# Kernel optimization log

Measured on AMD Instinct MI355X. Metric: run time of the kernel, lower is better.

The kernel has to match this reference:

```python
import jax, jax.numpy as jnp
import numpy as np

NUM_BOXES = 16384
NUM_CLASS = 3
CODE_SIZE = 7
NMS_PRE = 1024
NMS_POST = 512
NMS_THRESH = 0.8
EPS = 1e-8


def _cross(a, b):
    return a[..., 0] * b[..., 1] - a[..., 1] * b[..., 0]


def _bev_corners(b5):
    # b5: (..., 5) = (cx, cy, dx, dy, ry) -> corners (..., 4, 2)
    c, s = jnp.cos(b5[..., 4]), jnp.sin(b5[..., 4])
    off = jnp.array([[0.5, 0.5], [-0.5, 0.5], [-0.5, -0.5], [0.5, -0.5]], dtype=b5.dtype)
    lx = b5[..., 2:3] * off[:, 0]  # (..., 4)
    ly = b5[..., 3:4] * off[:, 1]
    cx = b5[..., 0:1] + lx * c[..., None] - ly * s[..., None]
    cy = b5[..., 1:2] + lx * s[..., None] + ly * c[..., None]
    return jnp.stack([cx, cy], axis=-1)


def _points_in_box(p, b5):
    # p: (..., K, 2), b5: (..., 5) -> (..., K) bool (point inside rotated rect)
    c, s = jnp.cos(b5[..., 4:5]), jnp.sin(b5[..., 4:5])
    rel = p - b5[..., None, 0:2]
    qx = rel[..., 0] * c + rel[..., 1] * s
    qy = -rel[..., 0] * s + rel[..., 1] * c
    return (jnp.abs(qx) <= b5[..., 2:3] * 0.5 + 1e-5) & (jnp.abs(qy) <= b5[..., 3:4] * 0.5 + 1e-5)


def _pairwise_bev_iou(b5):
    # b5: (N, 5) -> (N, N) rotated BEV IoU (matches iou3d nms_gpu's BEV IoU)
    a = b5[:, None, :]
    b = b5[None, :, :]
    ca = _bev_corners(a)  # (N,1,4,2)
    cb = _bev_corners(b)  # (1,N,4,2)
    # edge-edge segment intersections: (N,N,4,4)
    a0, da = ca, jnp.roll(ca, -1, axis=-2) - ca
    b0, db = cb, jnp.roll(cb, -1, axis=-2) - cb
    A0, DA = a0[..., :, None, :], da[..., :, None, :]
    B0, DB = b0[..., None, :, :], db[..., None, :, :]
    den = _cross(DA, DB)
    d = B0 - A0
    den_s = jnp.where(jnp.abs(den) > EPS, den, 1.0)
    t = _cross(d, DB) / den_s
    u = _cross(d, DA) / den_s
    ok = (jnp.abs(den) > EPS) & (t >= 0) & (t <= 1) & (u >= 0) & (u <= 1)
    p_ee = A0 + t[..., None] * DA  # (N,N,4,4,2)
    shp = p_ee.shape[:-3]
    p_ee = p_ee.reshape(shp + (16, 2))
    ok = ok.reshape(shp + (16,))
    in_b = _points_in_box(ca, b)  # corners of A inside B: (N,N,4)
    in_a = _points_in_box(cb, a)  # corners of B inside A: (N,N,4)
    pts = jnp.concatenate([p_ee,
                           jnp.broadcast_to(ca, shp + (4, 2)),
                           jnp.broadcast_to(cb, shp + (4, 2))], axis=-2)  # (N,N,24,2)
    msk = jnp.concatenate([ok, in_b, in_a], axis=-1)  # (N,N,24)
    # order candidate vertices by angle around centroid (intersection is convex)
    cnt = jnp.maximum(msk.sum(-1, keepdims=True), 1)
    ctr = (pts * msk[..., None]).sum(-2, keepdims=True) / cnt[..., None]  # (N,N,1,2)
    ang = jnp.arctan2(pts[..., 1] - ctr[..., 1], pts[..., 0] - ctr[..., 0])
    ang = jnp.where(msk, ang, 1e9)  # invalid points sorted to the end
    order = jnp.argsort(ang, axis=-1)
    pts_s = jnp.take_along_axis(pts, order[..., None], axis=-2)
    msk_s = jnp.take_along_axis(msk, order, axis=-1)
    first = pts_s[..., 0:1, :]
    poly = jnp.where(msk_s[..., None], pts_s, first)  # pad with first vertex (zero shoelace contribution)
    inter = 0.5 * jnp.abs(_cross(poly, jnp.roll(poly, -1, axis=-2)).sum(-1))
    area_a = a[..., 2] * a[..., 3]
    area_b = b[..., 2] * b[..., 3]
    return inter / jnp.maximum(area_a + area_b - inter, 1e-6)


def _greedy_nms(iou, thresh):
    n = iou.shape[0]
    idx = jnp.arange(n)

    def body(i, supp):
        alive = jnp.logical_not(supp[i])
        return supp | (alive & (iou[i] > thresh) & (idx > i))

    supp = jax.lax.fori_loop(0, n, body, jnp.zeros((n,), dtype=bool))
    return ~supp


def _select_one(box_preds, cls_preds):
    # box_preds: (M, 7), cls_preds: (M, C) -> padded selected indices + validity
    scores = jnp.max(cls_preds, axis=1)
    _, top_idx = jax.lax.top_k(scores, NMS_PRE)  # score-descending, like torch.topk
    bev = box_preds[top_idx][:, jnp.array([0, 1, 3, 4, 6])]  # (cx,cy,dx,dy,ry)
    iou = _pairwise_bev_iou(bev)
    keep = _greedy_nms(iou, NMS_THRESH)
    pri = jnp.where(keep, jnp.arange(NMS_PRE), 2 * NMS_PRE)
    pos = jnp.sort(pri)[:NMS_POST]  # kept positions in score order
    valid = pos < NMS_PRE
    sel = top_idx[jnp.minimum(pos, NMS_PRE - 1)]
    return sel, valid


def setup_inputs() -> dict:
    key = jax.random.key(0)
    k1, k2, k3, k4, k5 = jax.random.split(key, 5)
    B = 2
    xy = jax.random.uniform(k1, (B, NUM_BOXES, 2), minval=-50.0, maxval=50.0)
    z = jax.random.uniform(k2, (B, NUM_BOXES, 1), minval=-2.0, maxval=1.0)
    dims = jax.random.uniform(k3, (B, NUM_BOXES, 3), minval=1.0, maxval=5.0)
    ry = jax.random.uniform(k4, (B, NUM_BOXES, 1), minval=-np.pi, maxval=np.pi)
    batch_box_preds = jnp.concatenate([xy, z, dims, ry], axis=-1).astype(jnp.float32)
    batch_cls_preds = (jax.random.normal(k5, (B, NUM_BOXES, NUM_CLASS)) * 3.0).astype(jnp.float32)
    return {"batch_box_preds": batch_box_preds, "batch_cls_preds": batch_cls_preds}


def reference(batch_box_preds, batch_cls_preds):
    # RoIHeadTemplate.proposal_layer: per-sample max-score, class-agnostic NMS,
    # scatter into zero-padded (B, NMS_POST, ...) tensors.
    sel, valid = jax.vmap(_select_one)(batch_box_preds, batch_cls_preds)  # (B, NMS_POST)
    rois = jnp.take_along_axis(batch_box_preds, sel[..., None], axis=1)
    logits = jnp.take_along_axis(batch_cls_preds, sel[..., None], axis=1)
    labels = jnp.argmax(logits, axis=-1)
    scores = jnp.max(logits, axis=-1)
    v = valid[..., None]
    rois = jnp.where(v, rois, 0.0)
    logits = jnp.where(v, logits, 0.0)
    scores = jnp.where(valid, scores, 0.0)
    roi_labels = jnp.where(valid, labels, 0) + 1  # padded slots end up as 1, same as torch (zeros + 1)
    return rois, scores, roi_labels, logits
```

## Files before the change

### kernel.cpp

```cpp
#include <hip/hip_runtime.h>
#include <hip/hip_bf16.h>
#include <math.h>

#define NBOX   16384
#define NPRE   1024
#define NPOST  512
#define NMS_TH 0.8f
#define DEN_EPS 1e-8f
#define NCAND  2048
#define NBUCK  8192

typedef unsigned long long ull;

__device__ __forceinline__ unsigned mono_f32(float a) {
  unsigned u = __float_as_uint(a);
  return (u & 0x80000000u) ? ~u : (u | 0x80000000u);
}

__global__ __launch_bounds__(1024) void k_hist(
    const float* __restrict__ cls, ull* __restrict__ cand,
    unsigned* __restrict__ candCount, unsigned* __restrict__ nz) {
  __shared__ unsigned hist[NBUCK];
  __shared__ unsigned wsuf[16];
  __shared__ unsigned thrT;
  __shared__ unsigned cnt;
  int b = blockIdx.x;
  int t = threadIdx.x;
  int lane = t & 63, wv = t >> 6;
  nz[b * NPRE + t] = 0u;
#pragma unroll
  for (int k = 0; k < NBUCK / 1024; ++k) hist[t + k * 1024] = 0u;
  if (t == 0) cnt = 0u;
  __syncthreads();

  ull key[16];
#pragma unroll
  for (int k = 0; k < 16; ++k) {
    int i = k * 1024 + t;
    const float* cc = cls + ((size_t)b * NBOX + i) * 3;
    float s = fmaxf(cc[0], fmaxf(cc[1], cc[2]));
    unsigned u = mono_f32(s);
    key[k] = ((ull)u << 14) | (ull)(16383 - i);
    atomicAdd(&hist[u >> 19], 1u);
  }
  __syncthreads();

  unsigned s8 = 0;
#pragma unroll
  for (int k = 0; k < 8; ++k) s8 += hist[t * 8 + k];
  unsigned v = s8;
#pragma unroll
  for (int off = 1; off < 64; off <<= 1) {
    unsigned o = __shfl_down(v, off, 64);
    if (lane + off < 64) v += o;
  }
  if (lane == 0) wsuf[wv] = v;
  __syncthreads();
  if (t < 16) {
    unsigned x = wsuf[t];
#pragma unroll
    for (int off = 1; off < 16; off <<= 1) {
      unsigned o = __shfl_down(x, off, 64);
      if (t + off < 16) x += o;
    }
    wsuf[t] = x;
  }
  __syncthreads();
  unsigned Sown = v + ((wv < 15) ? wsuf[wv + 1] : 0u);
  unsigned Snxt = Sown - s8;
  if (Sown >= NPRE && Snxt < NPRE) {
    unsigned c = Snxt;
    unsigned T = t * 8;
    for (int k = 7; k >= 0; --k) {
      c += hist[t * 8 + k];
      if (c >= NPRE) { T = t * 8 + k; break; }
    }
    thrT = T;
  }
  __syncthreads();
  unsigned T = thrT;
#pragma unroll
  for (int k = 0; k < 16; ++k) {
    bool c = (unsigned)(key[k] >> 33) >= T;
    ull bal = __ballot(c);
    if (bal) {
      unsigned base = 0;
      if (lane == 0) base = atomicAdd(&cnt, (unsigned)__popcll(bal));
      base = (unsigned)__shfl((int)base, 0, 64);
      if (c) {
        unsigned pos = base + (unsigned)__popcll(bal & ((1ull << lane) - 1ull));
        if (pos < NCAND) cand[(size_t)b * NCAND + pos] = key[k];
      }
    }
  }
  __syncthreads();
  if (t == 0) candCount[b] = (cnt < NCAND) ? cnt : NCAND;
}

__global__ __launch_bounds__(256) void k_ranksel(
    const float* __restrict__ box, const ull* __restrict__ cand,
    const unsigned* __restrict__ candCount,
    int* __restrict__ topi, float* __restrict__ binfo, float4* __restrict__ pinfo) {
  __shared__ ull lk[NCAND];
  int b = blockIdx.y;
  int tid = threadIdx.x;
  int j = blockIdx.x * 256 + tid;
  unsigned C = candCount[b];
#pragma unroll
  for (int k = 0; k < NCAND / 256; ++k) {
    int idx = k * 256 + tid;
    lk[idx] = ((unsigned)idx < C) ? cand[(size_t)b * NCAND + idx] : 0ULL;
  }
  __syncthreads();
  ull my = ((unsigned)j < C) ? lk[j] : 0ULL;
  int r = 0;
  const ulonglong2* p2 = (const ulonglong2*)lk;
#pragma unroll 8
  for (int k = 0; k < NCAND / 2; ++k) {
    ulonglong2 kk = p2[k];
    r += (kk.x > my) ? 1 : 0;
    r += (kk.y > my) ? 1 : 0;
  }
  if ((unsigned)j >= C || r >= NPRE) return;
  int i = 16383 - (int)(my & 0x3FFFULL);
  topi[b * NPRE + r] = i;
  const float* bp = box + ((size_t)b * NBOX + i) * 7;
  float x = bp[0], y = bp[1], dx = bp[3], dy = bp[4], ry = bp[6];
  float c = cosf(ry), s = sinf(ry);
  float* o = binfo + ((size_t)b * NPRE + r) * 16;
  o[0] = x; o[1] = y; o[2] = dx; o[3] = dy; o[4] = c; o[5] = s;
  const float offx[4] = {0.5f, -0.5f, -0.5f, 0.5f};
  const float offy[4] = {0.5f, 0.5f, -0.5f, -0.5f};
#pragma unroll
  for (int k = 0; k < 4; ++k) {
    float lx = dx * offx[k], ly = dy * offy[k];
    o[6 + k]  = x + lx * c - ly * s;
    o[10 + k] = y + lx * s + ly * c;
  }
  float rad = 0.5f * sqrtf(dx * dx + dy * dy);
  float area = dx * dy;
  o[14] = rad; o[15] = area;
  pinfo[(size_t)b * NPRE + r] = make_float4(x, y, rad, area);
}

__device__ bool iou_exact_gt(const float* __restrict__ Ab, const float* __restrict__ Bb) {
  float ax = Ab[0], ay = Ab[1], bx = Bb[0], by = Bb[1];
  float aA = Ab[15], aB = Bb[15];
  float acx[4], acy[4], bcx[4], bcy[4];
#pragma unroll
  for (int k = 0; k < 4; ++k) {
    acx[k] = Ab[6 + k]; acy[k] = Ab[10 + k];
    bcx[k] = Bb[6 + k]; bcy[k] = Bb[10 + k];
  }
  float px[24], py[24];
  bool act[24];
#pragma unroll
  for (int p = 0; p < 4; ++p) {
    float A0x = acx[p], A0y = acy[p];
    float DAx = acx[(p + 1) & 3] - A0x, DAy = acy[(p + 1) & 3] - A0y;
#pragma unroll
    for (int q = 0; q < 4; ++q) {
      float B0x = bcx[q], B0y = bcy[q];
      float DBx = bcx[(q + 1) & 3] - B0x, DBy = bcy[(q + 1) & 3] - B0y;
      float den = DAx * DBy - DAy * DBx;
      float dxx = B0x - A0x, dyy = B0y - A0y;
      bool dok = fabsf(den) > DEN_EPS;
      float dens = dok ? den : 1.0f;
      float t = (dxx * DBy - dyy * DBx) / dens;
      float u = (dxx * DAy - dyy * DAx) / dens;
      int k = p * 4 + q;
      px[k] = A0x + t * DAx;
      py[k] = A0y + t * DAy;
      act[k] = dok && t >= 0.f && t <= 1.f && u >= 0.f && u <= 1.f;
    }
  }
  float cA = Ab[4], sA = Ab[5], cB = Bb[4], sB = Bb[5];
#pragma unroll
  for (int k = 0; k < 4; ++k) {
    float rx = acx[k] - bx, ry = acy[k] - by;
    float qx =  rx * cB + ry * sB, qy = -rx * sB + ry * cB;
    px[16 + k] = acx[k]; py[16 + k] = acy[k];
    act[16 + k] = (fabsf(qx) <= Bb[2] * 0.5f + 1e-5f) && (fabsf(qy) <= Bb[3] * 0.5f + 1e-5f);
  }
#pragma unroll
  for (int k = 0; k < 4; ++k) {
    float rx = bcx[k] - ax, ry = bcy[k] - ay;
    float qx =  rx * cA + ry * sA, qy = -rx * sA + ry * cA;
    px[20 + k] = bcx[k]; py[20 + k] = bcy[k];
    act[20 + k] = (fabsf(qx) <= Ab[2] * 0.5f + 1e-5f) && (fabsf(qy) <= Ab[3] * 0.5f + 1e-5f);
  }
  int cnt = 0; float sx = 0.f, sy = 0.f;
#pragma unroll
  for (int k = 0; k < 24; ++k)
    if (act[k]) { cnt++; sx += px[k]; sy += py[k]; }
  float fc = (float)(cnt > 1 ? cnt : 1);
  float cx0 = sx / fc, cy0 = sy / fc;
  ull key[24];
#pragma unroll
  for (int k = 0; k < 24; ++k) {
    float ang = atan2f(py[k] - cy0, px[k] - cx0);
    key[k] = act[k] ? ((((ull)mono_f32(ang)) << 5) | (ull)k) : ~0ull;
  }
  ull kmin = ~0ull; float fx = 0.f, fy = 0.f;
#pragma unroll
  for (int k = 0; k < 24; ++k) {
    bool lt = key[k] < kmin;
    kmin = lt ? key[k] : kmin;
    fx = lt ? px[k] : fx;
    fy = lt ? py[k] : fy;
  }
  float ssum = 0.f;
#pragma unroll
  for (int k = 0; k < 24; ++k) {
    ull myk = key[k];
    ull best = ~0ull; float nx = fx, ny = fy;
#pragma unroll
    for (int j = 0; j < 24; ++j) {
      bool c = (key[j] > myk) && (key[j] < best);
      best = c ? key[j] : best;
      nx = c ? px[j] : nx;
      ny = c ? py[j] : ny;
    }
    float contrib = px[k] * ny - py[k] * nx;
    ssum += (myk != ~0ull) ? contrib : 0.f;
  }
  float inter = 0.5f * fabsf(ssum);
  float uni = aA + aB - inter;
  return inter / fmaxf(uni, 1e-6f) > NMS_TH;
}

__global__ __launch_bounds__(256) void k_pairs(
    const float* __restrict__ binfo, const float4* __restrict__ pinfo,
    ull* __restrict__ mask, unsigned* __restrict__ nz) {
  int wv = (blockIdx.x * 256 + threadIdx.x) >> 6;
  int lane = threadIdx.x & 63;
  int w = wv & 15;
  int i = (wv >> 4) & (NPRE - 1);
  int b = wv >> 14;
  if (w * 64 + 63 <= i) return;
  int j = w * 64 + lane;
  float4 pj = pinfo[(size_t)b * NPRE + j];
  float4 pi = pinfo[(size_t)b * NPRE + i];
  bool cand = false;
  if (j > i) {
    float ddx = pi.x - pj.x, ddy = pi.y - pj.y;
    float rr = pi.z + pj.z + 1e-3f;
    if (ddx * ddx + ddy * ddy <= rr * rr) {
      float mn = fminf(pi.w, pj.w), mx = fmaxf(pi.w, pj.w);
      if (mn > NMS_TH * mx) cand = true;
    }
  }
  const float* base = binfo + (size_t)b * NPRE * 16;
  bool pred = cand && iou_exact_gt(base + (size_t)i * 16, base + (size_t)j * 16);
  ull bal = __ballot(pred);
  if (lane == 0 && bal) {
    mask[((size_t)b * NPRE + i) * 16 + w] = bal;
    atomicOr(&nz[b * NPRE + i], 1u << w);
  }
}

__global__ __launch_bounds__(1024) void k_final(
    const float* __restrict__ box, const float* __restrict__ cls,
    const int* __restrict__ topi, const ull* __restrict__ mask,
    const unsigned* __restrict__ nz, float* __restrict__ out, int B) {
  __shared__ ull remv_sh[16];
  int b = blockIdx.x;
  int p = threadIdx.x;
  int lane = p & 63, wid = p >> 6;

  if (wid == 0) {
    ull rfr[16];
#pragma unroll
    for (int w = 0; w < 16; ++w) {
      unsigned vz = nz[b * NPRE + w * 64 + lane];
      rfr[w] = __ballot(vz != 0u);
    }
    ull remv = 0;
    for (int w = 0; w < 16; ++w) {
      ull bb = rfr[w];
      while (bb) {
        int ii = __ffsll(bb) - 1;
        bb &= bb - 1;
        int row = w * 64 + ii;
        ull rw = __shfl(remv, w, 64);
        if (!((rw >> ii) & 1ULL)) {
          unsigned nzi = nz[b * NPRE + row];
          ull m = 0;
          if (lane < 16 && ((nzi >> lane) & 1u))
            m = mask[((size_t)b * NPRE + row) * 16 + lane];
          remv |= m;
        }
      }
    }
    if (lane < 16) remv_sh[lane] = remv;
  }
  __syncthreads();

  ull rw = remv_sh[wid];
  int alive = ((rw >> lane) & 1ULL) ? 0 : 1;
  int v = alive;
#pragma unroll
  for (int off = 1; off < 64; off <<= 1) {
    int t = __shfl_up(v, off, 64);
    if (lane >= off) v += t;
  }
  __shared__ int wtot[16], woff[17];
  if (lane == 63) wtot[wid] = v;
  __syncthreads();
  if (p == 0) {
    int acc = 0;
    for (int t = 0; t < 16; ++t) { woff[t] = acc; acc += wtot[t]; }
    woff[16] = acc;
  }
  __syncthreads();
  int excl = v - alive + woff[wid];
  int total = woff[16];
  float* rois   = out;
  float* scores = out + (size_t)B * NPOST * 7;
  float* labels = scores + (size_t)B * NPOST;
  float* logits = labels + (size_t)B * NPOST;
  if (alive && excl < NPOST) {
    int s = excl;
    int orig = topi[b * NPRE + p];
    const float* bb = box + ((size_t)b * NBOX + orig) * 7;
    float* ro = rois + ((size_t)b * NPOST + s) * 7;
#pragma unroll
    for (int c = 0; c < 7; ++c) ro[c] = bb[c];
    const float* cc = cls + ((size_t)b * NBOX + orig) * 3;
    float l0 = cc[0], l1 = cc[1], l2 = cc[2];
    float m = fmaxf(l0, fmaxf(l1, l2));
    int lab = (l0 == m) ? 0 : ((l1 == m) ? 1 : 2);
    scores[b * NPOST + s] = m;
    labels[b * NPOST + s] = (float)(lab + 1);
    float* lg = logits + ((size_t)b * NPOST + s) * 3;
    lg[0] = l0; lg[1] = l1; lg[2] = l2;
  }
  if (p < NPOST && p >= total) {
    float* ro = rois + ((size_t)b * NPOST + p) * 7;
#pragma unroll
    for (int c = 0; c < 7; ++c) ro[c] = 0.f;
    scores[b * NPOST + p] = 0.f;
    labels[b * NPOST + p] = 1.f;
    float* lg = logits + ((size_t)b * NPOST + p) * 3;
    lg[0] = 0.f; lg[1] = 0.f; lg[2] = 0.f;
  }
}

extern "C" void kernel_launch(void* const* d_in, const int* in_sizes, int n_in,
                              void* d_out, int out_size, void* d_ws, size_t ws_size,
                              hipStream_t stream) {
  const float* box = (const float*)d_in[0];
  const float* cls = (const float*)d_in[1];
  float* out = (float*)d_out;
  int B = in_sizes[0] / (NBOX * 7);

  char* w = (char*)d_ws;
  size_t off = 0;
  ull* cand        = (ull*)(w + off);      off += (size_t)B * NCAND * sizeof(ull);
  unsigned* candCt = (unsigned*)(w + off); off += (size_t)B * sizeof(unsigned);
  int* topi        = (int*)(w + off);      off += (size_t)B * NPRE * sizeof(int);
  off = (off + 63) & ~(size_t)63;
  float* binfo     = (float*)(w + off);    off += (size_t)B * NPRE * 16 * sizeof(float);
  float4* pinfo    = (float4*)(w + off);   off += (size_t)B * NPRE * sizeof(float4);
  ull* mask        = (ull*)(w + off);      off += (size_t)B * NPRE * 16 * sizeof(ull);
  unsigned* nz     = (unsigned*)(w + off); off += (size_t)B * NPRE * sizeof(unsigned);
  (void)off; (void)ws_size; (void)out_size; (void)n_in;

  hipLaunchKernelGGL(k_hist,    dim3(B), dim3(1024), 0, stream, cls, cand, candCt, nz);
  hipLaunchKernelGGL(k_ranksel, dim3(NCAND / 256, B), dim3(256), 0, stream, box, cand, candCt, topi, binfo, pinfo);
  hipLaunchKernelGGL(k_pairs,   dim3(B * NPRE * 16 / 4), dim3(256), 0, stream, binfo, pinfo, mask, nz);
  hipLaunchKernelGGL(k_final,   dim3(B), dim3(1024), 0, stream, box, cls, topi, mask, nz, out, B);
}
```

Before: 157.7 us.

## Fuse top-k, rank-select and pair prefilter into one kernel with worklist NMS

Merges histogram threshold, rank selection and the coarse pair prefilter into a single per-sample kernel. Candidate keys and pinfo now stay in LDS, and pairs that pass the prefilter go to a compact global worklist. The final kernel evaluates exact IoU only on worklist pairs, builds a compact suppression mask in LDS for rows that hit, then runs the serial NMS scan and output scatter. This removes two launches, the dense per-row mask array and the global candidate round trip. The cost is that work now runs on only B blocks, which may serialize the IoU evaluation onto few CUs.

```diff
diff --git a/kernel.cpp b/kernel.cpp
--- a/kernel.cpp
+++ b/kernel.cpp
@@ -9,6 +9,9 @@
 #define DEN_EPS 1e-8f
 #define NCAND  2048
 #define NBUCK  8192
+#define WCAP_B (1u << 20)
+#define HITS_LDS 2048
+#define HSPILL  (1u << 19)
 
 typedef unsigned long long ull;
 
@@ -17,28 +20,30 @@
   return (u & 0x80000000u) ? ~u : (u | 0x80000000u);
 }
 
-__global__ __launch_bounds__(1024) void k_hist(
-    const float* __restrict__ cls, ull* __restrict__ cand,
-    unsigned* __restrict__ candCount, unsigned* __restrict__ nz) {
+__global__ __launch_bounds__(1024) void k_topk(
+    const float* __restrict__ box, const float* __restrict__ cls,
+    int* __restrict__ topi, float* __restrict__ binfo,
+    unsigned* __restrict__ wl, unsigned* __restrict__ wcnt) {
   __shared__ unsigned hist[NBUCK];
+  ull*    candL  = (ull*)hist;
+  float4* pinfoL = (float4*)&hist[4096];
   __shared__ unsigned wsuf[16];
-  __shared__ unsigned thrT;
-  __shared__ unsigned cnt;
-  int b = blockIdx.x;
-  int t = threadIdx.x;
-  int lane = t & 63, wv = t >> 6;
-  nz[b * NPRE + t] = 0u;
+  __shared__ unsigned thrT, cntC, cntW;
+
+  const int b = blockIdx.x, t = threadIdx.x;
+  const int lane = t & 63, wv = t >> 6;
+
 #pragma unroll
   for (int k = 0; k < NBUCK / 1024; ++k) hist[t + k * 1024] = 0u;
-  if (t == 0) cnt = 0u;
+  if (t == 0) { cntC = 0u; cntW = 0u; }
   __syncthreads();
 
   ull key[16];
+  const float* cb = cls + (size_t)b * NBOX * 3;
 #pragma unroll
   for (int k = 0; k < 16; ++k) {
     int i = k * 1024 + t;
-    const float* cc = cls + ((size_t)b * NBOX + i) * 3;
-    float s = fmaxf(cc[0], fmaxf(cc[1], cc[2]));
+    float s = fmaxf(cb[i * 3], fmaxf(cb[i * 3 + 1], cb[i * 3 + 2]));
     unsigned u = mono_f32(s);
     key[k] = ((ull)u << 14) | (ull)(16383 - i);
     atomicAdd(&hist[u >> 19], 1u);
@@ -51,7 +56,7 @@
   unsigned v = s8;
 #pragma unroll
   for (int off = 1; off < 64; off <<= 1) {
-    unsigned o = __shfl_down(v, off, 64);
+    unsigned o = __shfl_down((int)v, off, 64);
     if (lane + off < 64) v += o;
   }
   if (lane == 0) wsuf[wv] = v;
@@ -60,7 +65,7 @@
     unsigned x = wsuf[t];
 #pragma unroll
     for (int off = 1; off < 16; off <<= 1) {
-      unsigned o = __shfl_down(x, off, 64);
+      unsigned o = __shfl_down((int)x, off, 64);
       if (t + off < 16) x += o;
     }
     wsuf[t] = x;
@@ -70,77 +75,105 @@
   unsigned Snxt = Sown - s8;
   if (Sown >= NPRE && Snxt < NPRE) {
     unsigned c = Snxt;
-    unsigned T = t * 8;
     for (int k = 7; k >= 0; --k) {
       c += hist[t * 8 + k];
-      if (c >= NPRE) { T = t * 8 + k; break; }
-    }
-    thrT = T;
+      if (c >= NPRE) { thrT = (unsigned)(t * 8 + k); break; }
+    }
   }
   __syncthreads();
   unsigned T = thrT;
+
 #pragma unroll
   for (int k = 0; k < 16; ++k) {
     bool c = (unsigned)(key[k] >> 33) >= T;
     ull bal = __ballot(c);
     if (bal) {
       unsigned base = 0;
-      if (lane == 0) base = atomicAdd(&cnt, (unsigned)__popcll(bal));
+      if (lane == 0) base = atomicAdd(&cntC, (unsigned)__popcll(bal));
       base = (unsigned)__shfl((int)base, 0, 64);
       if (c) {
         unsigned pos = base + (unsigned)__popcll(bal & ((1ull << lane) - 1ull));
-        if (pos < NCAND) cand[(size_t)b * NCAND + pos] = key[k];
+        if (pos < NCAND) candL[pos] = key[k];
       }
     }
   }
   __syncthreads();
-  if (t == 0) candCount[b] = (cnt < NCAND) ? cnt : NCAND;
-}
-
-__global__ __launch_bounds__(256) void k_ranksel(
-    const float* __restrict__ box, const ull* __restrict__ cand,
-    const unsigned* __restrict__ candCount,
-    int* __restrict__ topi, float* __restrict__ binfo, float4* __restrict__ pinfo) {
-  __shared__ ull lk[NCAND];
-  int b = blockIdx.y;
-  int tid = threadIdx.x;
-  int j = blockIdx.x * 256 + tid;
-  unsigned C = candCount[b];
-#pragma unroll
-  for (int k = 0; k < NCAND / 256; ++k) {
-    int idx = k * 256 + tid;
-    lk[idx] = ((unsigned)idx < C) ? cand[(size_t)b * NCAND + idx] : 0ULL;
-  }
-  __syncthreads();
-  ull my = ((unsigned)j < C) ? lk[j] : 0ULL;
-  int r = 0;
-  const ulonglong2* p2 = (const ulonglong2*)lk;
-#pragma unroll 8
-  for (int k = 0; k < NCAND / 2; ++k) {
+  unsigned C = cntC; if (C > NCAND) C = NCAND;
+  if (t < 2 && C + t < NCAND) candL[C + t] = 0ull;
+  __syncthreads();
+
+  ull my1 = (2u * t     < C) ? candL[2 * t]     : 0ull;
+  ull my2 = (2u * t + 1 < C) ? candL[2 * t + 1] : 0ull;
+  int r1 = 0, r2 = 0;
+  int kmax = (int)((C + 1) >> 1);
+  const ulonglong2* p2 = (const ulonglong2*)candL;
+  for (int k = 0; k < kmax; ++k) {
     ulonglong2 kk = p2[k];
-    r += (kk.x > my) ? 1 : 0;
-    r += (kk.y > my) ? 1 : 0;
-  }
-  if ((unsigned)j >= C || r >= NPRE) return;
-  int i = 16383 - (int)(my & 0x3FFFULL);
-  topi[b * NPRE + r] = i;
-  const float* bp = box + ((size_t)b * NBOX + i) * 7;
-  float x = bp[0], y = bp[1], dx = bp[3], dy = bp[4], ry = bp[6];
-  float c = cosf(ry), s = sinf(ry);
-  float* o = binfo + ((size_t)b * NPRE + r) * 16;
-  o[0] = x; o[1] = y; o[2] = dx; o[3] = dy; o[4] = c; o[5] = s;
-  const float offx[4] = {0.5f, -0.5f, -0.5f, 0.5f};
-  const float offy[4] = {0.5f, 0.5f, -0.5f, -0.5f};
-#pragma unroll
-  for (int k = 0; k < 4; ++k) {
-    float lx = dx * offx[k], ly = dy * offy[k];
-    o[6 + k]  = x + lx * c - ly * s;
-    o[10 + k] = y + lx * s + ly * c;
-  }
-  float rad = 0.5f * sqrtf(dx * dx + dy * dy);
-  float area = dx * dy;
-  o[14] = rad; o[15] = area;
-  pinfo[(size_t)b * NPRE + r] = make_float4(x, y, rad, area);
+    r1 += (kk.x > my1) ? 1 : 0; r1 += (kk.y > my1) ? 1 : 0;
+    r2 += (kk.x > my2) ? 1 : 0; r2 += (kk.y > my2) ? 1 : 0;
+  }
+
+  const float* boxb = box + (size_t)b * NBOX * 7;
+#pragma unroll
+  for (int sl = 0; sl < 2; ++sl) {
+    ull my = sl ? my2 : my1;
+    int r  = sl ? r2  : r1;
+    bool valid = (2u * t + sl < C) && (r < NPRE);
+    if (valid) {
+      int i = 16383 - (int)(my & 0x3FFFULL);
+      topi[b * NPRE + r] = i;
+      const float* bp = boxb + (size_t)i * 7;
+      float x = bp[0], y = bp[1], dx = bp[3], dy = bp[4], ry = bp[6];
+      float c = cosf(ry), s = sinf(ry);
+      float* o = binfo + ((size_t)b * NPRE + r) * 16;
+      o[0] = x; o[1] = y; o[2] = dx; o[3] = dy; o[4] = c; o[5] = s;
+      const float offx[4] = {0.5f, -0.5f, -0.5f, 0.5f};
+      const float offy[4] = {0.5f, 0.5f, -0.5f, -0.5f};
+#pragma unroll
+      for (int k = 0; k < 4; ++k) {
+        float lx = dx * offx[k], ly = dy * offy[k];
+        o[6 + k]  = x + lx * c - ly * s;
+        o[10 + k] = y + lx * s + ly * c;
+      }
+      float rad = 0.5f * sqrtf(dx * dx + dy * dy);
+      float area = dx * dy;
+      o[14] = rad; o[15] = area;
+      pinfoL[r] = make_float4(x, y, rad, area);
+    }
+  }
+  __syncthreads();
+
+  unsigned wbase = (unsigned)b * WCAP_B;
+  for (int q = 0; q < 64; ++q) {
+    int i = q * 16 + wv;
+    float4 pi = pinfoL[i];
+#pragma unroll
+    for (int w2 = 0; w2 < 16; ++w2) {
+      if (w2 * 64 + 63 <= i) continue;
+      int j = w2 * 64 + lane;
+      float4 pj = pinfoL[j];
+      bool cnd = false;
+      if (j > i) {
+        float ddx = pi.x - pj.x, ddy = pi.y - pj.y;
+        float rr = pi.z + pj.z + 1e-3f;
+        if (ddx * ddx + ddy * ddy <= rr * rr) {
+          float mn = fminf(pi.w, pj.w), mx = fmaxf(pi.w, pj.w);
+          if (mn > NMS_TH * mx) cnd = true;
+        }
+      }
+      ull bal = __ballot(cnd);
+      if (!bal) continue;
+      unsigned base = 0;
+      if (lane == 0) base = atomicAdd(&cntW, (unsigned)__popcll(bal));
+      base = (unsigned)__shfl((int)base, 0, 64);
+      if (cnd) {
+        unsigned off = base + (unsigned)__popcll(bal & ((1ull << lane) - 1ull));
+        if (off < WCAP_B) wl[wbase + off] = ((unsigned)i << 10) | (unsigned)j;
+      }
+    }
+  }
+  __syncthreads();
+  if (t == 0) wcnt[b] = (cntW < WCAP_B) ? cntW : WCAP_B;
 }
 
 __device__ bool iou_exact_gt(const float* __restrict__ Ab, const float* __restrict__ Bb) {
@@ -229,119 +262,142 @@
   return inter / fmaxf(uni, 1e-6f) > NMS_TH;
 }
 
-__global__ __launch_bounds__(256) void k_pairs(
-    const float* __restrict__ binfo, const float4* __restrict__ pinfo,
-    ull* __restrict__ mask, unsigned* __restrict__ nz) {
-  int wv = (blockIdx.x * 256 + threadIdx.x) >> 6;
-  int lane = threadIdx.x & 63;
-  int w = wv & 15;
-  int i = (wv >> 4) & (NPRE - 1);
-  int b = wv >> 14;
-  if (w * 64 + 63 <= i) return;
-  int j = w * 64 + lane;
-  float4 pj = pinfo[(size_t)b * NPRE + j];
-  float4 pi = pinfo[(size_t)b * NPRE + i];
-  bool cand = false;
-  if (j > i) {
-    float ddx = pi.x - pj.x, ddy = pi.y - pj.y;
-    float rr = pi.z + pj.z + 1e-3f;
-    if (ddx * ddx + ddy * ddy <= rr * rr) {
-      float mn = fminf(pi.w, pj.w), mx = fmaxf(pi.w, pj.w);
-      if (mn > NMS_TH * mx) cand = true;
-    }
-  }
-  const float* base = binfo + (size_t)b * NPRE * 16;
-  bool pred = cand && iou_exact_gt(base + (size_t)i * 16, base + (size_t)j * 16);
-  ull bal = __ballot(pred);
-  if (lane == 0 && bal) {
-    mask[((size_t)b * NPRE + i) * 16 + w] = bal;
-    atomicOr(&nz[b * NPRE + i], 1u << w);
-  }
-}
-
-__global__ __launch_bounds__(1024) void k_final(
+__device__ __forceinline__ int popbelow(const unsigned* rowbm, int i) {
+  int s = 0, w = i >> 5;
+  for (int k = 0; k < w; ++k) s += __popc(rowbm[k]);
+  s += __popc(rowbm[w] & ((1u << (i & 31)) - 1u));
+  return s;
+}
+
+__global__ __launch_bounds__(512) void k_final(
     const float* __restrict__ box, const float* __restrict__ cls,
-    const int* __restrict__ topi, const ull* __restrict__ mask,
-    const unsigned* __restrict__ nz, float* __restrict__ out, int B) {
+    const int* __restrict__ topi, const float* __restrict__ binfo,
+    const unsigned* __restrict__ wl, const unsigned* __restrict__ wcnt,
+    unsigned* __restrict__ hspill, float* __restrict__ out, int B) {
+  __shared__ unsigned maskL[128 * 32];
+  __shared__ unsigned hitsL[HITS_LDS];
+  __shared__ unsigned rlist[NPRE];
+  __shared__ unsigned rowbm[32];
   __shared__ ull remv_sh[16];
-  int b = blockIdx.x;
-  int p = threadIdx.x;
-  int lane = p & 63, wid = p >> 6;
-
-  if (wid == 0) {
-    ull rfr[16];
-#pragma unroll
-    for (int w = 0; w < 16; ++w) {
-      unsigned vz = nz[b * NPRE + w * 64 + lane];
-      rfr[w] = __ballot(vz != 0u);
-    }
+  __shared__ unsigned smallu[8];
+  __shared__ unsigned hcnt, rn_sh;
+
+  const int b = blockIdx.x, t = threadIdx.x;
+  const int lane = t & 63, wv = t >> 6;
+
+  for (int k = t; k < 128 * 32; k += 512) maskL[k] = 0u;
+  if (t < 32) rowbm[t] = 0u;
+  if (t == 0) hcnt = 0u;
+  __syncthreads();
+
+  const float* bi = binfo + (size_t)b * NPRE * 16;
+  unsigned n = wcnt[b]; if (n > WCAP_B) n = WCAP_B;
+  for (unsigned e = (unsigned)t; e < n; e += 512) {
+    unsigned pk = wl[(size_t)b * WCAP_B + e];
+    unsigned i = pk >> 10, j = pk & 1023u;
+    if (iou_exact_gt(bi + (size_t)i * 16, bi + (size_t)j * 16)) {
+      unsigned h = atomicAdd(&hcnt, 1u);
+      if (h < HITS_LDS) hitsL[h] = pk;
+      else if (h < HITS_LDS + HSPILL) hspill[(size_t)b * HSPILL + (h - HITS_LDS)] = pk;
+      atomicOr(&rowbm[i >> 5], 1u << (i & 31));
+    }
+  }
+  __syncthreads();
+
+  for (int row = t; row < NPRE; row += 512) {
+    if ((rowbm[row >> 5] >> (row & 31)) & 1u)
+      rlist[popbelow(rowbm, row)] = (unsigned)row;
+  }
+  if (t == 0) {
+    unsigned s = 0;
+    for (int w = 0; w < 32; ++w) s += (unsigned)__popc(rowbm[w]);
+    rn_sh = s;
+  }
+  __syncthreads();
+  unsigned H = hcnt; if (H > HITS_LDS + HSPILL) H = HITS_LDS + HSPILL;
+  for (unsigned h = (unsigned)t; h < H; h += 512) {
+    unsigned pk = (h < HITS_LDS) ? hitsL[h] : hspill[(size_t)b * HSPILL + (h - HITS_LDS)];
+    unsigned i = pk >> 10, j = pk & 1023u;
+    int slot = popbelow(rowbm, (int)i);
+    if (slot < 128) atomicOr(&maskL[slot * 32 + (j >> 5)], 1u << (j & 31));
+  }
+  __syncthreads();
+
+  if (wv == 0) {
     ull remv = 0;
-    for (int w = 0; w < 16; ++w) {
-      ull bb = rfr[w];
-      while (bb) {
-        int ii = __ffsll(bb) - 1;
-        bb &= bb - 1;
-        int row = w * 64 + ii;
-        ull rw = __shfl(remv, w, 64);
-        if (!((rw >> ii) & 1ULL)) {
-          unsigned nzi = nz[b * NPRE + row];
-          ull m = 0;
-          if (lane < 16 && ((nzi >> lane) & 1u))
-            m = mask[((size_t)b * NPRE + row) * 16 + lane];
-          remv |= m;
+    unsigned rn = rn_sh;
+    for (unsigned s = 0; s < rn; ++s) {
+      unsigned row = rlist[s];
+      ull m = 0;
+      if (s < 128) {
+        if (lane < 16)
+          m = (ull)maskL[s * 32 + lane * 2] | ((ull)maskL[s * 32 + lane * 2 + 1] << 32);
+      } else {
+        for (unsigned h = 0; h < H; ++h) {
+          unsigned pk = (h < HITS_LDS) ? hitsL[h] : hspill[(size_t)b * HSPILL + (h - HITS_LDS)];
+          if ((pk >> 10) == row) {
+            unsigned j = pk & 1023u;
+            if (lane == (int)(j >> 6)) m |= 1ull << (j & 63);
+          }
         }
       }
+      ull rw = __shfl(remv, (int)(row >> 6), 64);
+      if (!((rw >> (row & 63)) & 1ULL)) remv |= m;
     }
     if (lane < 16) remv_sh[lane] = remv;
   }
   __syncthreads();
 
-  ull rw = remv_sh[wid];
-  int alive = ((rw >> lane) & 1ULL) ? 0 : 1;
-  int v = alive;
+  int p0 = t * 2;
+  ull rw = remv_sh[p0 >> 6];
+  int a0 = ((rw >> (p0 & 63)) & 1ULL) ? 0 : 1;
+  int a1 = ((rw >> ((p0 + 1) & 63)) & 1ULL) ? 0 : 1;
+  int myc = a0 + a1;
+  int v = myc;
 #pragma unroll
   for (int off = 1; off < 64; off <<= 1) {
-    int t = __shfl_up(v, off, 64);
-    if (lane >= off) v += t;
-  }
-  __shared__ int wtot[16], woff[17];
-  if (lane == 63) wtot[wid] = v;
-  __syncthreads();
-  if (p == 0) {
-    int acc = 0;
-    for (int t = 0; t < 16; ++t) { woff[t] = acc; acc += wtot[t]; }
-    woff[16] = acc;
-  }
-  __syncthreads();
-  int excl = v - alive + woff[wid];
-  int total = woff[16];
+    int t2 = __shfl_up(v, off, 64);
+    if (lane >= off) v += t2;
+  }
+  if (lane == 63) smallu[wv] = (unsigned)v;
+  __syncthreads();
+  int pre = 0;
+  for (int w2 = 0; w2 < wv; ++w2) pre += (int)smallu[w2];
+  int total = 0;
+  for (int w2 = 0; w2 < 8; ++w2) total += (int)smallu[w2];
+  int s = pre + v - myc;
+
   float* rois   = out;
   float* scores = out + (size_t)B * NPOST * 7;
   float* labels = scores + (size_t)B * NPOST;
   float* logits = labels + (size_t)B * NPOST;
-  if (alive && excl < NPOST) {
-    int s = excl;
-    int orig = topi[b * NPRE + p];
-    const float* bb = box + ((size_t)b * NBOX + orig) * 7;
-    float* ro = rois + ((size_t)b * NPOST + s) * 7;
-#pragma unroll
-    for (int c = 0; c < 7; ++c) ro[c] = bb[c];
-    const float* cc = cls + ((size_t)b * NBOX + orig) * 3;
-    float l0 = cc[0], l1 = cc[1], l2 = cc[2];
-    float m = fmaxf(l0, fmaxf(l1, l2));
-    int lab = (l0 == m) ? 0 : ((l1 == m) ? 1 : 2);
-    scores[b * NPOST + s] = m;
-    labels[b * NPOST + s] = (float)(lab + 1);
-    float* lg = logits + ((size_t)b * NPOST + s) * 3;
-    lg[0] = l0; lg[1] = l1; lg[2] = l2;
-  }
-  if (p < NPOST && p >= total) {
-    float* ro = rois + ((size_t)b * NPOST + p) * 7;
-#pragma unroll
-    for (int c = 0; c < 7; ++c) ro[c] = 0.f;
-    scores[b * NPOST + p] = 0.f;
-    labels[b * NPOST + p] = 1.f;
-    float* lg = logits + ((size_t)b * NPOST + p) * 3;
+  int aa[2] = {a0, a1};
+#pragma unroll
+  for (int k = 0; k < 2; ++k) {
+    if (aa[k] && s < NPOST) {
+      int orig = topi[b * NPRE + p0 + k];
+      const float* bb = box + ((size_t)b * NBOX + orig) * 7;
+      float* ro = rois + ((size_t)b * NPOST + s) * 7;
+#pragma unroll
+      for (int c2 = 0; c2 < 7; ++c2) ro[c2] = bb[c2];
+      const float* cc = cls + ((size_t)b * NBOX + orig) * 3;
+      float l0 = cc[0], l1 = cc[1], l2 = cc[2];
+      float m = fmaxf(l0, fmaxf(l1, l2));
+      int lab = (l0 == m) ? 0 : ((l1 == m) ? 1 : 2);
+      scores[b * NPOST + s] = m;
+      labels[b * NPOST + s] = (float)(lab + 1);
+      float* lg = logits + ((size_t)b * NPOST + s) * 3;
+      lg[0] = l0; lg[1] = l1; lg[2] = l2;
+    }
+    s += aa[k];
+  }
+  if (t < NPOST && t >= total) {
+    float* ro = rois + ((size_t)b * NPOST + t) * 7;
+#pragma unroll
+    for (int c2 = 0; c2 < 7; ++c2) ro[c2] = 0.f;
+    scores[b * NPOST + t] = 0.f;
+    labels[b * NPOST + t] = 1.f;
+    float* lg = logits + ((size_t)b * NPOST + t) * 3;
     lg[0] = 0.f; lg[1] = 0.f; lg[2] = 0.f;
   }
 }
@@ -356,18 +412,14 @@
 
   char* w = (char*)d_ws;
   size_t off = 0;
-  ull* cand        = (ull*)(w + off);      off += (size_t)B * NCAND * sizeof(ull);
-  unsigned* candCt = (unsigned*)(w + off); off += (size_t)B * sizeof(unsigned);
   int* topi        = (int*)(w + off);      off += (size_t)B * NPRE * sizeof(int);
+  unsigned* wcnt   = (unsigned*)(w + off); off += 64;
   off = (off + 63) & ~(size_t)63;
   float* binfo     = (float*)(w + off);    off += (size_t)B * NPRE * 16 * sizeof(float);
-  float4* pinfo    = (float4*)(w + off);   off += (size_t)B * NPRE * sizeof(float4);
-  ull* mask        = (ull*)(w + off);      off += (size_t)B * NPRE * 16 * sizeof(ull);
-  unsigned* nz     = (unsigned*)(w + off); off += (size_t)B * NPRE * sizeof(unsigned);
+  unsigned* wl     = (unsigned*)(w + off); off += (size_t)B * WCAP_B * sizeof(unsigned);
+  unsigned* hspill = (unsigned*)(w + off); off += (size_t)B * HSPILL * sizeof(unsigned);
   (void)off; (void)ws_size; (void)out_size; (void)n_in;
 
-  hipLaunchKernelGGL(k_hist,    dim3(B), dim3(1024), 0, stream, cls, cand, candCt, nz);
-  hipLaunchKernelGGL(k_ranksel, dim3(NCAND / 256, B), dim3(256), 0, stream, box, cand, candCt, topi, binfo, pinfo);
-  hipLaunchKernelGGL(k_pairs,   dim3(B * NPRE * 16 / 4), dim3(256), 0, stream, binfo, pinfo, mask, nz);
-  hipLaunchKernelGGL(k_final,   dim3(B), dim3(1024), 0, stream, box, cls, topi, mask, nz, out, B);
-}
+  hipLaunchKernelGGL(k_topk,  dim3(B), dim3(1024), 0, stream, box, cls, topi, binfo, wl, wcnt);
+  hipLaunchKernelGGL(k_final, dim3(B), dim3(512),  0, stream, box, cls, topi, binfo, wl, wcnt, hspill, out, B);
+}
```

After: 240.3 us. +52.4%, slower.
